# Kernel optimization log

Hardware: AMD Instinct MI355X
Metric: run time of the kernel (lower is better)

Reference implementation:

```python
import jax, jax.numpy as jnp
import numpy as np

B, N, C_IN, C_OUT, H = 8, 1024, 256, 512, 8
DH = C_OUT // H  # per-head dim
LN_EPS = 1e-5


def setup_inputs() -> dict:
    key = jax.random.key(0)
    ks = jax.random.split(key, 8)
    # xavier_normal std for [in, out] fan pair
    std = float(np.sqrt(2.0 / (C_IN + DH)))
    x = jax.random.normal(ks[0], (B, N, C_IN), dtype=jnp.float32)
    adj = jax.random.uniform(ks[1], (B, N, N), dtype=jnp.float32)
    W_q = jax.random.normal(ks[2], (H, C_IN, DH), dtype=jnp.float32) * std
    W_k = jax.random.normal(ks[3], (H, C_IN, DH), dtype=jnp.float32) * std
    W_v = jax.random.normal(ks[4], (H, C_IN, DH), dtype=jnp.float32) * std
    # Conv1d(in, out, kernel=1) == pointwise linear: weight [out, in], bias [out]
    bound = float(1.0 / np.sqrt(C_IN))
    conv_w = jax.random.uniform(ks[5], (C_OUT, C_IN), dtype=jnp.float32, minval=-bound, maxval=bound)
    conv_b = jax.random.uniform(ks[6], (C_OUT,), dtype=jnp.float32, minval=-bound, maxval=bound)
    ln_w = jnp.ones((C_OUT,), dtype=jnp.float32)
    ln_b = jnp.zeros((C_OUT,), dtype=jnp.float32)
    return {"x": x, "adj": adj, "W_q": W_q, "W_k": W_k, "W_v": W_v,
            "conv_w": conv_w, "conv_b": conv_b, "ln_w": ln_w, "ln_b": ln_b}


def reference(x, adj, W_q, W_k, W_v, conv_w, conv_b, ln_w, ln_b):
    # NOTE: in the original module, adj is used only to compute D_neg/A_hat,
    # which are discarded; it has no effect on the output. Attention is dense.
    dh = W_q.shape[-1]
    scale = 1.0 / jnp.sqrt(jnp.asarray(dh, dtype=x.dtype))
    # batched per-head projections: [B,N,Cin] x [H,Cin,dh] -> [B,H,N,dh]
    Q = jnp.einsum('bni,hio->bhno', x, W_q)
    K = jnp.einsum('bni,hio->bhno', x, W_k)
    V = jnp.einsum('bni,hio->bhno', x, W_v)
    scores = jnp.einsum('bhqd,bhkd->bhqk', Q, K) * scale  # [B,H,N,N]
    attn = jax.nn.softmax(scores, axis=-1)
    out = jax.nn.relu(jnp.einsum('bhqk,bhkd->bhqd', attn, V))  # [B,H,N,dh]
    b, h, n, d = out.shape
    out = out.transpose(0, 2, 1, 3).reshape(b, n, h * d)  # concat heads -> [B,N,Cout]
    # matching_conv: 1x1 conv == linear over channels
    proj = jnp.einsum('bni,oi->bno', x, conv_w) + conv_b
    y = out + proj
    mean = jnp.mean(y, axis=-1, keepdims=True)
    var = jnp.var(y, axis=-1, keepdims=True)
    y = (y - mean) * jax.lax.rsqrt(var + LN_EPS)
    return y * ln_w + ln_b
```

## Files before the change

kernel.cpp:

```cpp
#include <hip/hip_runtime.h>

#define B_ 8
#define N_ 1024
#define CIN_ 256
#define COUT_ 512
#define H_ 8
#define DH_ 64

typedef __attribute__((ext_vector_type(8))) short bf8;
typedef __attribute__((ext_vector_type(4))) short s4;
typedef __attribute__((ext_vector_type(4))) float f4;
typedef __attribute__((ext_vector_type(2))) unsigned int u2;

__device__ __forceinline__ short f2bf(float f) {
  unsigned u = __builtin_bit_cast(unsigned, f);
  u += 0x7fffu + ((u >> 16) & 1u);
  return (short)(u >> 16);
}
__device__ __forceinline__ float bf2f(short s) {
  unsigned u = ((unsigned)(unsigned short)s) << 16;
  return __builtin_bit_cast(float, u);
}

#if __has_builtin(__builtin_amdgcn_exp2f)
#define EXP2 __builtin_amdgcn_exp2f
#else
#define EXP2 exp2f
#endif

__device__ __forceinline__ unsigned cvtpk(float a, float b) {
  unsigned u;
  asm("v_cvt_pk_bf16_f32 %0, %1, %2" : "=v"(u) : "v"(a), "v"(b));
  return u;
}

#define MFMA16(a, b, c) __builtin_amdgcn_mfma_f32_16x16x32_bf16((a), (b), (c), 0, 0, 0)

#define GLD16(gp, lp)                                                              \
  __builtin_amdgcn_global_load_lds((const __attribute__((address_space(1))) void*)(gp), \
                                   (__attribute__((address_space(3))) void*)(lp), 16, 0, 0)

__global__ void k_prep(const float* __restrict__ Wq, const float* __restrict__ Wk,
                       const float* __restrict__ Wv, const float* __restrict__ Cw,
                       const float* __restrict__ x, short* __restrict__ Wt,
                       short* __restrict__ xb) {
  int blk = blockIdx.x;
  if (blk < 2048) {
    int col = blk;
    int k = threadIdx.x;
    float v;
    if (col < 512) {
      int h = col >> 6, d = col & 63;
      v = Wq[(h * CIN_ + k) * DH_ + d];
    } else if (col < 1024) {
      int c = col - 512, h = c >> 6, d = c & 63;
      v = Wk[(h * CIN_ + k) * DH_ + d];
    } else if (col < 1536) {
      int c = col - 1024, h = c >> 6, d = c & 63;
      v = Wv[(h * CIN_ + k) * DH_ + d];
    } else {
      v = Cw[(col - 1536) * CIN_ + k];
    }
    Wt[col * CIN_ + k] = f2bf(v);
  } else {
    int i = (blk - 2048) * 256 + threadIdx.x;
    f4 a = *reinterpret_cast<const f4*>(x + (size_t)i * 8);
    f4 b = *reinterpret_cast<const f4*>(x + (size_t)i * 8 + 4);
    bf8 o;
    o[0] = f2bf(a[0]); o[1] = f2bf(a[1]); o[2] = f2bf(a[2]); o[3] = f2bf(a[3]);
    o[4] = f2bf(b[0]); o[5] = f2bf(b[1]); o[6] = f2bf(b[2]); o[7] = f2bf(b[3]);
    *reinterpret_cast<bf8*>(xb + (size_t)i * 8) = o;
  }
}

__global__ __launch_bounds__(256) void k_gemm(const short* __restrict__ xb, const short* __restrict__ Wt,
                                              short* __restrict__ Qw, short* __restrict__ Kw,
                                              short* __restrict__ Vt, short* __restrict__ Pj) {
  __shared__ short Al[128][72];
  __shared__ short Bl[128][72];
  int tid = threadIdx.x;
  int mt = blockIdx.x >> 4, nt = blockIdx.x & 15;
  int row0 = mt * 128, col0 = nt * 128;
  int w = tid >> 6, lane = tid & 63, g = lane >> 4, lr = lane & 15;
  int wm = w >> 1, wn = w & 1;
  f4 acc[4][4];
#pragma unroll
  for (int i = 0; i < 4; ++i)
#pragma unroll
    for (int j = 0; j < 4; ++j) acc[i][j] = (f4){0.f, 0.f, 0.f, 0.f};

  int r_st = tid >> 3, c_st = tid & 7;
  for (int kt = 0; kt < 4; ++kt) {
    int k0 = kt * 64;
#pragma unroll
    for (int i = 0; i < 4; ++i) {
      int r = r_st + i * 32;
      bf8 va = *reinterpret_cast<const bf8*>(xb + (row0 + r) * CIN_ + k0 + c_st * 8);
      bf8 vb = *reinterpret_cast<const bf8*>(Wt + (col0 + r) * CIN_ + k0 + c_st * 8);
      *reinterpret_cast<bf8*>(&Al[r][c_st * 8]) = va;
      *reinterpret_cast<bf8*>(&Bl[r][c_st * 8]) = vb;
    }
    __syncthreads();
    bf8 af[4][2], bb[4][2];
#pragma unroll
    for (int mi = 0; mi < 4; ++mi) {
      af[mi][0] = *reinterpret_cast<const bf8*>(&Al[wm * 64 + mi * 16 + lr][g * 8]);
      af[mi][1] = *reinterpret_cast<const bf8*>(&Al[wm * 64 + mi * 16 + lr][32 + g * 8]);
    }
#pragma unroll
    for (int ni = 0; ni < 4; ++ni) {
      bb[ni][0] = *reinterpret_cast<const bf8*>(&Bl[wn * 64 + ni * 16 + lr][g * 8]);
      bb[ni][1] = *reinterpret_cast<const bf8*>(&Bl[wn * 64 + ni * 16 + lr][32 + g * 8]);
    }
#pragma unroll
    for (int mi = 0; mi < 4; ++mi)
#pragma unroll
      for (int ni = 0; ni < 4; ++ni) {
        acc[mi][ni] = MFMA16(af[mi][0], bb[ni][0], acc[mi][ni]);
        acc[mi][ni] = MFMA16(af[mi][1], bb[ni][1], acc[mi][ni]);
      }
    __syncthreads();
  }
  const float QSCL = 0.125f * 1.4426950408889634f;
#pragma unroll
  for (int mi = 0; mi < 4; ++mi)
#pragma unroll
    for (int ni = 0; ni < 4; ++ni) {
      int c = col0 + wn * 64 + ni * 16 + lr;
      int r0 = row0 + wm * 64 + mi * 16 + g * 4;
      int b = r0 >> 10, n0 = r0 & 1023;
      if (c < 1024) {
#pragma unroll
        for (int j = 0; j < 4; ++j) {
          int n = n0 + j;
          if (c < 512) {
            Qw[((b * H_ + (c >> 6)) * N_ + n) * DH_ + (c & 63)] = f2bf(acc[mi][ni][j] * QSCL);
          } else {
            int cc = c - 512;
            Kw[((b * H_ + (cc >> 6)) * N_ + n) * DH_ + (cc & 63)] = f2bf(acc[mi][ni][j]);
          }
        }
      } else if (c < 1536) {
        int cc = c - 1024;
        int hh = cc >> 6, d = cc & 63;
        s4 vv;
#pragma unroll
        for (int j = 0; j < 4; ++j) vv[j] = f2bf(acc[mi][ni][j]);
        *reinterpret_cast<s4*>(Vt + ((size_t)(b * H_ + hh) * DH_ + d) * N_ + n0) = vv;
      } else {
#pragma unroll
        for (int j = 0; j < 4; ++j) {
          Pj[(size_t)(r0 + j) * COUT_ + (c - 1536)] = f2bf(acc[mi][ni][j]);
        }
      }
    }
}

__global__ __launch_bounds__(256) void k_attn(const short* __restrict__ Qw, const short* __restrict__ Kw,
                                              const short* __restrict__ Vt, short* __restrict__ At) {
  __shared__ short Kl[2][64][64];
  __shared__ short Vl[2][64][64];
  __shared__ short Pl[4][2][16][64];
  int tid = threadIdx.x;
  int nid = ((blockIdx.x & 7) << 6) | (blockIdx.x >> 3);
  int bh = nid >> 3;
  int qb = nid & 7;
  int w = tid >> 6, lane = tid & 63, g = lane >> 4, lr = lane & 15;
  int qglob = qb * 128 + w * 32;
  const short* Qp = Qw + ((size_t)bh * N_ + qglob) * DH_;
  const short* Kp = Kw + (size_t)bh * N_ * DH_;
  const short* Vp = Vt + (size_t)bh * DH_ * N_;

  int sr0 = tid >> 3, sc0 = (tid & 7) ^ (sr0 & 7);
  int s1 = tid + 256;
  int sr1 = s1 >> 3, sc1 = (s1 & 7) ^ (sr1 & 7);
  int lo0 = (w * 64) << 4;
  int lo1 = (w * 64 + 256) << 4;

  {
    const short* kb = Kp;
    const short* vb = Vp;
    char* klb = (char*)&Kl[0][0][0];
    char* vlb = (char*)&Vl[0][0][0];
    GLD16(kb + sr0 * 64 + sc0 * 8, klb + lo0);
    GLD16(kb + sr1 * 64 + sc1 * 8, klb + lo1);
    GLD16(vb + (size_t)sr0 * N_ + sc0 * 8, vlb + lo0);
    GLD16(vb + (size_t)sr1 * N_ + sc1 * 8, vlb + lo1);
  }

  bf8 aq[2][2];
#pragma unroll
  for (int qs = 0; qs < 2; ++qs) {
    aq[qs][0] = *reinterpret_cast<const bf8*>(Qp + (qs * 16 + lr) * DH_ + g * 8);
    aq[qs][1] = *reinterpret_cast<const bf8*>(Qp + (qs * 16 + lr) * DH_ + 32 + g * 8);
  }

  f4 o[2][4];
  f4 lacc[2];
#pragma unroll
  for (int qs = 0; qs < 2; ++qs) {
    lacc[qs] = (f4){0.f, 0.f, 0.f, 0.f};
#pragma unroll
    for (int i = 0; i < 4; ++i) o[qs][i] = (f4){0.f, 0.f, 0.f, 0.f};
  }

  const int swz = (lr & 7) << 3;
  short* pl0 = &Pl[w][0][0][0];
  short* pl1 = &Pl[w][1][0][0];

  for (int t = 0; t < 16; ++t) {
    int cur = t & 1;
    if (t < 15) {
      const short* kb = Kp + (t + 1) * (64 * DH_);
      const short* vb = Vp + (t + 1) * 64;
      char* klb = (char*)&Kl[cur ^ 1][0][0];
      char* vlb = (char*)&Vl[cur ^ 1][0][0];
      GLD16(kb + sr0 * 64 + sc0 * 8, klb + lo0);
      GLD16(kb + sr1 * 64 + sc1 * 8, klb + lo1);
      GLD16(vb + (size_t)sr0 * N_ + sc0 * 8, vlb + lo0);
      GLD16(vb + (size_t)sr1 * N_ + sc1 * 8, vlb + lo1);
      asm volatile("s_waitcnt vmcnt(4)" ::: "memory");
    } else {
      asm volatile("s_waitcnt vmcnt(0)" ::: "memory");
    }
    __builtin_amdgcn_s_barrier();

    const short* klc = &Kl[cur][0][0];
    bf8 bk0[4], bk1[4];
#pragma unroll
    for (int kt = 0; kt < 4; ++kt) {
      int R = kt * 16 + lr;
      const short* kr = klc + R * 64;
      int sw = (R & 7) << 3;
      bk0[kt] = *reinterpret_cast<const bf8*>(kr + ((g * 8) ^ sw));
      bk1[kt] = *reinterpret_cast<const bf8*>(kr + ((32 + g * 8) ^ sw));
    }
    f4 s0[4], s1v[4];
#pragma unroll
    for (int kt = 0; kt < 4; ++kt) {
      f4 z = (f4){0.f, 0.f, 0.f, 0.f};
      z = MFMA16(bk0[kt], aq[0][0], z);
      z = MFMA16(bk1[kt], aq[0][1], z);
      s0[kt] = z;
      f4 z2 = (f4){0.f, 0.f, 0.f, 0.f};
      z2 = MFMA16(bk0[kt], aq[1][0], z2);
      z2 = MFMA16(bk1[kt], aq[1][1], z2);
      s1v[kt] = z2;
    }
#pragma unroll
    for (int kt = 0; kt < 4; ++kt) {
      f4 p;
      p[0] = EXP2(s0[kt][0]); p[1] = EXP2(s0[kt][1]);
      p[2] = EXP2(s0[kt][2]); p[3] = EXP2(s0[kt][3]);
      lacc[0] += p;
      u2 pk;
      pk[0] = cvtpk(p[0], p[1]);
      pk[1] = cvtpk(p[2], p[3]);
      *reinterpret_cast<u2*>(pl0 + lr * 64 + ((kt * 16 + g * 4) ^ swz)) = pk;
    }
#pragma unroll
    for (int kt = 0; kt < 4; ++kt) {
      f4 p;
      p[0] = EXP2(s1v[kt][0]); p[1] = EXP2(s1v[kt][1]);
      p[2] = EXP2(s1v[kt][2]); p[3] = EXP2(s1v[kt][3]);
      lacc[1] += p;
      u2 pk;
      pk[0] = cvtpk(p[0], p[1]);
      pk[1] = cvtpk(p[2], p[3]);
      *reinterpret_cast<u2*>(pl1 + lr * 64 + ((kt * 16 + g * 4) ^ swz)) = pk;
    }
    asm volatile("s_waitcnt lgkmcnt(0)" ::: "memory");
    __builtin_amdgcn_sched_barrier(0);
    bf8 pa00 = *reinterpret_cast<const bf8*>(pl0 + lr * 64 + ((g * 8) ^ swz));
    bf8 pa01 = *reinterpret_cast<const bf8*>(pl0 + lr * 64 + ((32 + g * 8) ^ swz));
    bf8 pa10 = *reinterpret_cast<const bf8*>(pl1 + lr * 64 + ((g * 8) ^ swz));
    bf8 pa11 = *reinterpret_cast<const bf8*>(pl1 + lr * 64 + ((32 + g * 8) ^ swz));
    const short* vlc = &Vl[cur][0][0];
#pragma unroll
    for (int dt = 0; dt < 4; ++dt) {
      int R = dt * 16 + lr;
      const short* vr = vlc + R * 64;
      int sw = (R & 7) << 3;
      bf8 bv0 = *reinterpret_cast<const bf8*>(vr + ((g * 8) ^ sw));
      bf8 bv1 = *reinterpret_cast<const bf8*>(vr + ((32 + g * 8) ^ sw));
      o[0][dt] = MFMA16(pa00, bv0, o[0][dt]);
      o[0][dt] = MFMA16(pa01, bv1, o[0][dt]);
      o[1][dt] = MFMA16(pa10, bv0, o[1][dt]);
      o[1][dt] = MFMA16(pa11, bv1, o[1][dt]);
    }
    asm volatile("s_waitcnt lgkmcnt(0)" ::: "memory");
    __builtin_amdgcn_s_barrier();
  }

  float ls[2];
#pragma unroll
  for (int qs = 0; qs < 2; ++qs) {
    float v = (lacc[qs][0] + lacc[qs][1]) + (lacc[qs][2] + lacc[qs][3]);
    v += __shfl_xor(v, 16, 64);
    v += __shfl_xor(v, 32, 64);
    ls[qs] = v;
  }
  float lf[2][4];
#pragma unroll
  for (int qs = 0; qs < 2; ++qs)
#pragma unroll
    for (int j = 0; j < 4; ++j)
      lf[qs][j] = __shfl(ls[qs], (lane & 48) + ((lane & 48) >> 2) + j, 64);
  int b = bh >> 3, h = bh & 7;
#pragma unroll
  for (int qs = 0; qs < 2; ++qs)
#pragma unroll
    for (int dt = 0; dt < 4; ++dt)
#pragma unroll
      for (int j = 0; j < 4; ++j) {
        float v = fmaxf(o[qs][dt][j] / lf[qs][j], 0.f);
        int n = qglob + qs * 16 + g * 4 + j;
        At[((size_t)b * N_ + n) * COUT_ + h * DH_ + dt * 16 + lr] = f2bf(v);
      }
}

__global__ __launch_bounds__(256) void k_ln(const short* __restrict__ At, const short* __restrict__ Pj,
                                            const float* __restrict__ cb, const float* __restrict__ lw,
                                            const float* __restrict__ lb, float* __restrict__ out) {
  int row = blockIdx.x * 4 + (threadIdx.x >> 6);
  int lane = threadIdx.x & 63;
  int c0 = lane * 8;
  bf8 a8 = *reinterpret_cast<const bf8*>(At + (size_t)row * COUT_ + c0);
  bf8 p8 = *reinterpret_cast<const bf8*>(Pj + (size_t)row * COUT_ + c0);
  float y[8];
  float sum = 0.f, sq = 0.f;
#pragma unroll
  for (int j = 0; j < 8; ++j) {
    float v = bf2f(a8[j]) + bf2f(p8[j]) + cb[c0 + j];
    y[j] = v;
    sum += v;
    sq += v * v;
  }
#pragma unroll
  for (int off = 1; off < 64; off <<= 1) {
    sum += __shfl_xor(sum, off, 64);
    sq += __shfl_xor(sq, off, 64);
  }
  float mean = sum * (1.f / 512.f);
  float var = sq * (1.f / 512.f) - mean * mean;
  float rstd = rsqrtf(var + 1e-5f);
  f4 o0, o1;
#pragma unroll
  for (int j = 0; j < 4; ++j) o0[j] = (y[j] - mean) * rstd * lw[c0 + j] + lb[c0 + j];
#pragma unroll
  for (int j = 0; j < 4; ++j) o1[j] = (y[4 + j] - mean) * rstd * lw[c0 + 4 + j] + lb[c0 + 4 + j];
  *reinterpret_cast<f4*>(out + (size_t)row * COUT_ + c0) = o0;
  *reinterpret_cast<f4*>(out + (size_t)row * COUT_ + c0 + 4) = o1;
}

extern "C" void kernel_launch(void* const* d_in, const int* in_sizes, int n_in,
                              void* d_out, int out_size, void* d_ws, size_t ws_size,
                              hipStream_t stream) {
  const float* x  = (const float*)d_in[0];
  const float* Wq = (const float*)d_in[2];
  const float* Wk = (const float*)d_in[3];
  const float* Wv = (const float*)d_in[4];
  const float* Cw = (const float*)d_in[5];
  const float* cb = (const float*)d_in[6];
  const float* lw = (const float*)d_in[7];
  const float* lb = (const float*)d_in[8];
  float* out = (float*)d_out;
  char* ws = (char*)d_ws;
  short* xb = (short*)(ws);
  short* Wt = (short*)(ws + (size_t)4194304);
  short* Qw = (short*)(ws + (size_t)5242880);
  short* Kw = (short*)(ws + (size_t)13631488);
  short* Vt = (short*)(ws + (size_t)22020096);
  short* Pj = (short*)(ws + (size_t)30408704);
  short* At = (short*)(ws + (size_t)38797312);

  hipLaunchKernelGGL(k_prep, dim3(3072), dim3(256), 0, stream, Wq, Wk, Wv, Cw, x, Wt, xb);
  hipLaunchKernelGGL(k_gemm, dim3(1024), dim3(256), 0, stream, xb, Wt, Qw, Kw, Vt, Pj);
  hipLaunchKernelGGL(k_attn, dim3(512), dim3(256), 0, stream, Qw, Kw, Vt, At);
  hipLaunchKernelGGL(k_ln, dim3(2048), dim3(256), 0, stream, At, Pj, cb, lw, lb, out);
}
```

Before: 66.41 us.

## Double-buffer projection GEMM tiles with direct global-to-LDS loads and XOR swizzle

The projection GEMM kernel now stages A and B tiles with direct global-to-LDS loads (GLD16) into double-buffered shared memory, so the next k-tile is prefetched while the current one is used by MFMAs. The padded LDS layout is replaced by an XOR swizzle on 16-byte column groups to avoid bank conflicts without padding. It depends on a GLD16 macro defined elsewhere and on hand-written waitcnt/barrier sequencing, which risks races if the counts are off. This is one of several kernels, so its effect on total time is limited.

```diff
diff --git a/kernel.cpp b/kernel.cpp
--- a/kernel.cpp
+++ b/kernel.cpp
@@ -76,8 +76,8 @@
 __global__ __launch_bounds__(256) void k_gemm(const short* __restrict__ xb, const short* __restrict__ Wt,
                                               short* __restrict__ Qw, short* __restrict__ Kw,
                                               short* __restrict__ Vt, short* __restrict__ Pj) {
-  __shared__ short Al[128][72];
-  __shared__ short Bl[128][72];
+  __shared__ short Al[2][128][64];
+  __shared__ short Bl[2][128][64];
   int tid = threadIdx.x;
   int mt = blockIdx.x >> 4, nt = blockIdx.x & 15;
   int row0 = mt * 128, col0 = nt * 128;
@@ -89,28 +89,54 @@
 #pragma unroll
     for (int j = 0; j < 4; ++j) acc[i][j] = (f4){0.f, 0.f, 0.f, 0.f};
 
-  int r_st = tid >> 3, c_st = tid & 7;
+  int srow[4], sgc[4];
+#pragma unroll
+  for (int p = 0; p < 4; ++p) {
+    int s = p * 256 + tid;
+    srow[p] = s >> 3;
+    sgc[p] = (s & 7) ^ (srow[p] & 7);
+  }
+
+#define STAGE_AB(k0_, buf_)                                                     \
+  {                                                                             \
+    char* abase = (char*)&Al[buf_][0][0];                                       \
+    char* bbase = (char*)&Bl[buf_][0][0];                                       \
+    _Pragma("unroll")                                                           \
+    for (int p = 0; p < 4; ++p) {                                               \
+      int lb = (p * 256 + w * 64) << 4;                                         \
+      GLD16(xb + (row0 + srow[p]) * CIN_ + (k0_) + sgc[p] * 8, abase + lb);     \
+      GLD16(Wt + (col0 + srow[p]) * CIN_ + (k0_) + sgc[p] * 8, bbase + lb);     \
+    }                                                                           \
+  }
+
+  STAGE_AB(0, 0);
+
   for (int kt = 0; kt < 4; ++kt) {
-    int k0 = kt * 64;
-#pragma unroll
-    for (int i = 0; i < 4; ++i) {
-      int r = r_st + i * 32;
-      bf8 va = *reinterpret_cast<const bf8*>(xb + (row0 + r) * CIN_ + k0 + c_st * 8);
-      bf8 vb = *reinterpret_cast<const bf8*>(Wt + (col0 + r) * CIN_ + k0 + c_st * 8);
-      *reinterpret_cast<bf8*>(&Al[r][c_st * 8]) = va;
-      *reinterpret_cast<bf8*>(&Bl[r][c_st * 8]) = vb;
-    }
-    __syncthreads();
+    int cur = kt & 1;
+    if (kt < 3) {
+      STAGE_AB((kt + 1) * 64, cur ^ 1);
+      asm volatile("s_waitcnt vmcnt(8)" ::: "memory");
+    } else {
+      asm volatile("s_waitcnt vmcnt(0)" ::: "memory");
+    }
+    __builtin_amdgcn_s_barrier();
+
+    const short* al = &Al[cur][0][0];
+    const short* bl = &Bl[cur][0][0];
     bf8 af[4][2], bb[4][2];
 #pragma unroll
     for (int mi = 0; mi < 4; ++mi) {
-      af[mi][0] = *reinterpret_cast<const bf8*>(&Al[wm * 64 + mi * 16 + lr][g * 8]);
-      af[mi][1] = *reinterpret_cast<const bf8*>(&Al[wm * 64 + mi * 16 + lr][32 + g * 8]);
+      int R = wm * 64 + mi * 16 + lr;
+      int sw = R & 7;
+      af[mi][0] = *reinterpret_cast<const bf8*>(al + R * 64 + ((g ^ sw) * 8));
+      af[mi][1] = *reinterpret_cast<const bf8*>(al + R * 64 + (((4 + g) ^ sw) * 8));
     }
 #pragma unroll
     for (int ni = 0; ni < 4; ++ni) {
-      bb[ni][0] = *reinterpret_cast<const bf8*>(&Bl[wn * 64 + ni * 16 + lr][g * 8]);
-      bb[ni][1] = *reinterpret_cast<const bf8*>(&Bl[wn * 64 + ni * 16 + lr][32 + g * 8]);
+      int R = wn * 64 + ni * 16 + lr;
+      int sw = R & 7;
+      bb[ni][0] = *reinterpret_cast<const bf8*>(bl + R * 64 + ((g ^ sw) * 8));
+      bb[ni][1] = *reinterpret_cast<const bf8*>(bl + R * 64 + (((4 + g) ^ sw) * 8));
     }
 #pragma unroll
     for (int mi = 0; mi < 4; ++mi)
@@ -119,8 +145,10 @@
         acc[mi][ni] = MFMA16(af[mi][0], bb[ni][0], acc[mi][ni]);
         acc[mi][ni] = MFMA16(af[mi][1], bb[ni][1], acc[mi][ni]);
       }
-    __syncthreads();
-  }
+    asm volatile("s_waitcnt lgkmcnt(0)" ::: "memory");
+    __builtin_amdgcn_s_barrier();
+  }
+
   const float QSCL = 0.125f * 1.4426950408889634f;
 #pragma unroll
   for (int mi = 0; mi < 4; ++mi)
```

New measurement: 66.08 us. About the same (-0.5%).
